# Kernel tuning notes

Hardware: AMD Instinct MI355X
Metric: run time of the kernel (lower is better)

The kernel has to match this reference:

```python
import jax, jax.numpy as jnp
import numpy as np

B, C, T, H = 16, 128, 128, 128


def setup_inputs() -> dict:
    key = jax.random.key(0)
    ks = jax.random.split(key, 9)
    inp = {
        "food_relation": jax.random.normal(ks[0], (B, C, H), jnp.float32),
        "thorn_relation": jax.random.normal(ks[1], (B, C, T, H), jnp.float32),
        "clone": jax.random.normal(ks[2], (B, C, H), jnp.float32),
        "clone_relation": jax.random.normal(ks[3], (B, C, C, H), jnp.float32),
        "thorn_mask": jax.random.randint(ks[4], (B, T), 0, 2, jnp.int32),
        "clone_mask": jax.random.randint(ks[5], (B, C), 0, 2, jnp.int32),
        # MLP(layer_num=1) == Linear(in, h) + activation (ReLU)
        "W_thorn": jax.random.normal(ks[6], (2 * H, H), jnp.float32) / np.sqrt(2 * H),
        "b_thorn": jnp.zeros((H,), jnp.float32),
        "W_clone": jax.random.normal(ks[7], (3 * H, H), jnp.float32) / np.sqrt(3 * H),
        "b_clone": jnp.zeros((H,), jnp.float32),
        "W_agg": jax.random.normal(ks[8], (4 * H, H), jnp.float32) / np.sqrt(4 * H),
        "b_agg": jnp.zeros((H,), jnp.float32),
    }
    return inp


def reference(food_relation, thorn_relation, clone, clone_relation,
              thorn_mask, clone_mask,
              W_thorn, b_thorn, W_clone, b_clone, W_agg, b_agg):
    b, c, h = clone.shape
    t = thorn_relation.shape[2]
    tm = thorn_mask.astype(clone.dtype)[:, None, :, None]  # (b,1,t,1)
    cm = clone_mask.astype(clone.dtype)[:, None, :, None]  # (b,1,c,1)

    # thorn branch: MLP(concat([clone_i, thorn_rel_ij], -1))
    # == clone @ W[:h] (broadcast over t) + rel @ W[h:], avoiding the big concat
    x = ((clone @ W_thorn[:h])[:, :, None, :]
         + jnp.einsum('bcth,hk->bctk', thorn_relation, W_thorn[h:])
         + b_thorn)  # (b,c,t,h)
    thorn_agg = jnp.max(jax.nn.relu(x) * tm, axis=2)  # (b,c,h)

    # clone branch: MLP(concat([clone_i, clone_j, clone_rel_ij], -1))
    y = ((clone @ W_clone[:h])[:, :, None, :]
         + (clone @ W_clone[h:2 * h])[:, None, :, :]
         + jnp.einsum('bcdh,hk->bcdk', clone_relation, W_clone[2 * h:])
         + b_clone)  # (b,c,c,h)
    clone_agg = jnp.max(jax.nn.relu(y) * cm, axis=2)  # (b,c,h)

    agg = jnp.concatenate([clone, food_relation, thorn_agg, clone_agg], axis=-1)  # (b,c,4h)
    return clone + jax.nn.relu(agg @ W_agg + b_agg)
```

## Files before the change

kernel.cpp:

```cpp
#include <hip/hip_runtime.h>

#define BB 16
#define CC 128
#define TT 128
#define HH 128
#define BC (BB*CC)

typedef __attribute__((ext_vector_type(8))) short bf16x8;
typedef __attribute__((ext_vector_type(4))) float f32x4;

__device__ __forceinline__ unsigned short f2bf(float f) {
  union { float f; unsigned u; } v; v.f = f;
  unsigned u = v.u;
  u += 0x7FFFu + ((u >> 16) & 1u);
  return (unsigned short)(u >> 16);
}

__device__ __forceinline__ bf16x8 pack8(f32x4 a, f32x4 b) {
  bf16x8 r;
  r[0] = (short)f2bf(a[0]); r[1] = (short)f2bf(a[1]);
  r[2] = (short)f2bf(a[2]); r[3] = (short)f2bf(a[3]);
  r[4] = (short)f2bf(b[0]); r[5] = (short)f2bf(b[1]);
  r[6] = (short)f2bf(b[2]); r[7] = (short)f2bf(b[3]);
  return r;
}

__device__ __forceinline__ float bf2f(unsigned short u) {
  union { unsigned u; float f; } v; v.u = ((unsigned)u) << 16; return v.f;
}

__global__ __launch_bounds__(256) void prep_kernel(
    const float* __restrict__ Wt, const float* __restrict__ Wc, const float* __restrict__ Wa,
    const float* __restrict__ clone, const float* __restrict__ food,
    const float* __restrict__ bt, const float* __restrict__ bcl,
    const int* __restrict__ tmask, const int* __restrict__ cmask,
    unsigned short* __restrict__ W2sw, unsigned short* __restrict__ Wcsw,
    unsigned short* __restrict__ WaggT,
    float* __restrict__ cpt, float* __restrict__ cp1, float* __restrict__ cj2,
    unsigned short* __restrict__ agg,
    int* __restrict__ tidx, int* __restrict__ tcnt,
    int* __restrict__ cidx, int* __restrict__ ccnt) {
  const int blk = blockIdx.x, tid = threadIdx.x;
  if (blk < 48) {
    int i = blk * 256 + tid;
    if (i < 2048) {
      int f = i >> 6, l = i & 63;
      int kt = f >> 3, n = f & 7;
      int ncol = n * 16 + (l & 15);
      int k0 = kt * 32 + (l >> 4) * 8;
      unsigned short o[8];
      #pragma unroll
      for (int e = 0; e < 8; ++e) o[e] = f2bf(Wt[(128 + k0 + e) * 128 + ncol]);
      *(uint4*)&W2sw[i * 8] = *(uint4*)o;
    } else if (i < 4096) {
      int j = i - 2048;
      int f = j >> 6, l = j & 63;
      int kt = f >> 3, n = f & 7;
      int ncol = n * 16 + (l & 15);
      int k0 = kt * 32 + (l >> 4) * 8;
      unsigned short o[8];
      #pragma unroll
      for (int e = 0; e < 8; ++e) o[e] = f2bf(Wc[(256 + k0 + e) * 128 + ncol]);
      *(uint4*)&Wcsw[j * 8] = *(uint4*)o;
    } else {
      int j = i - 4096;
      int n = j >> 6, k0 = (j & 63) * 8;
      unsigned short o[8];
      #pragma unroll
      for (int e = 0; e < 8; ++e) o[e] = f2bf(Wa[(k0 + e) * 128 + n]);
      *(uint4*)&WaggT[n * 512 + k0] = *(uint4*)o;
    }
  } else if (blk < 304) {
    const int bc0 = (blk - 48) * 8;
    __shared__ float cl[8][128];
    for (int i = tid; i < 1024; i += 256) cl[i >> 7][i & 127] = clone[bc0 * 128 + i];
    __syncthreads();
    const int k = tid & 127, r0 = (tid >> 7) * 4;
    float s1[4], s2[4], s3[4];
    #pragma unroll
    for (int r = 0; r < 4; ++r) { s1[r] = bt[k]; s2[r] = bcl[k]; s3[r] = 0.f; }
    #pragma unroll 4
    for (int h = 0; h < 128; ++h) {
      float w1 = Wt[h * 128 + k], w2 = Wc[h * 128 + k], w3 = Wc[(128 + h) * 128 + k];
      #pragma unroll
      for (int r = 0; r < 4; ++r) {
        float c = cl[r0 + r][h];
        s1[r] = fmaf(c, w1, s1[r]);
        s2[r] = fmaf(c, w2, s2[r]);
        s3[r] = fmaf(c, w3, s3[r]);
      }
    }
    #pragma unroll
    for (int r = 0; r < 4; ++r) {
      cpt[(bc0 + r0 + r) * 128 + k] = s1[r];
      cp1[(bc0 + r0 + r) * 128 + k] = s2[r];
      cj2[(bc0 + r0 + r) * 128 + k] = s3[r];
    }
    for (int i = tid; i < 1024; i += 256) {
      int r = i >> 7, kk = i & 127;
      agg[(size_t)(bc0 + r) * 512 + kk]       = f2bf(cl[r][kk]);
      agg[(size_t)(bc0 + r) * 512 + 128 + kk] = f2bf(food[bc0 * 128 + i]);
    }
  } else {
    if (tid < 32) {
      int b = tid >> 1, which = tid & 1;
      const int* m = which ? cmask : tmask;
      int* idx = which ? cidx : tidx;
      int c = 0;
      for (int i = 0; i < 128; ++i)
        if (m[b * 128 + i]) idx[b * 128 + c++] = i;
      if (which) ccnt[b] = c; else tcnt[b] = c;
    }
  }
}

__global__ __launch_bounds__(512, 4) void branch13(
    const float* __restrict__ trel, const float* __restrict__ crel,
    const float* __restrict__ cpt, const float* __restrict__ cp1,
    const float* __restrict__ cj2,
    const int* __restrict__ tidx, const int* __restrict__ tcnt,
    const int* __restrict__ cidx, const int* __restrict__ ccnt,
    const uint4* __restrict__ W2sw, const uint4* __restrict__ Wcsw,
    unsigned short* __restrict__ agg) {
  __shared__ uint4 Wlds[32 * 64];
  __shared__ unsigned short cj2l[128][130];
  __shared__ int idxl[128];

  const bool isClone = blockIdx.x < 256;
  const int tileIdx = blockIdx.x & 255;
  const float* __restrict__ rel     = isClone ? crel  : trel;
  const float* __restrict__ biasrow = isClone ? cp1   : cpt;
  const int*   __restrict__ idxg    = isClone ? cidx  : tidx;
  const uint4* __restrict__ Wsw     = isClone ? Wcsw  : W2sw;
  const int aggoff = isClone ? 384 : 256;

  const int tid = threadIdx.x;
  const int wave = tid >> 6, lane = tid & 63;
  const int l16 = lane & 15, lk = lane >> 4;
  const int bc0 = tileIdx << 3;
  const int b = bc0 >> 7;
  const int cnt = (isClone ? ccnt : tcnt)[b];
  const int cl  = cnt > 0 ? cnt : 1;

  for (int i = tid; i < 2048; i += 512) Wlds[i] = Wsw[i];
  if (tid < 128) idxl[tid] = idxg[b * 128 + tid];
  if (isClone) {
    const float* cg = cj2 + (size_t)b * 128 * 128;
    for (int i = tid; i < 2048; i += 512) {
      int r = i >> 4, c8 = (i & 15) * 8;
      f32x4 a0 = *(const f32x4*)(cg + r * 128 + c8);
      f32x4 a1 = *(const f32x4*)(cg + r * 128 + c8 + 4);
      bf16x8 p = pack8(a0, a1);
      #pragma unroll
      for (int e = 0; e < 8; ++e) cj2l[c8 + e][r] = (unsigned short)p[e];
    }
  }
  __syncthreads();

  const int bc = bc0 + wave;
  const float* Rb = rel + (size_t)bc * 16384 + lk * 8;

  float bias[8];
  #pragma unroll
  for (int n = 0; n < 8; ++n) bias[n] = biasrow[bc * 128 + n * 16 + l16];

  float vmax[8];
  #pragma unroll
  for (int n = 0; n < 8; ++n) vmax[n] = 0.f;

  #pragma unroll 1
  for (int rg = 0; rg < 8; ++rg) {
    if ((rg << 4) < cnt) {
      int rs = (rg << 4) + l16; if (rs >= cl) rs = cl - 1;
      const float* Rt = Rb + idxl[rs] * 128;
      bf16x8 afr[4];
      #pragma unroll
      for (int kt = 0; kt < 4; ++kt)
        afr[kt] = pack8(*(const f32x4*)(Rt + kt * 32),
                        *(const f32x4*)(Rt + kt * 32 + 4));

      f32x4 acc[8];
      #pragma unroll
      for (int n = 0; n < 8; ++n) acc[n] = (f32x4){0.f, 0.f, 0.f, 0.f};
      #pragma unroll
      for (int kt = 0; kt < 4; ++kt) {
        #pragma unroll
        for (int n = 0; n < 8; ++n) {
          bf16x8 bfr = *(const bf16x8*)&Wlds[(kt * 8 + n) * 64 + lane];
          acc[n] = __builtin_amdgcn_mfma_f32_16x16x32_bf16(afr[kt], bfr, acc[n], 0, 0, 0);
        }
      }

      if (isClone) {
        int rowj[4];
        #pragma unroll
        for (int j = 0; j < 4; ++j) {
          int rj = (rg << 4) + lk * 4 + j; if (rj >= cl) rj = cl - 1;
          rowj[j] = idxl[rj];
        }
        #pragma unroll
        for (int n = 0; n < 8; ++n) {
          const int col = n * 16 + l16;
          #pragma unroll
          for (int j = 0; j < 4; ++j) {
            float x = acc[n][j] + bias[n] + bf2f(cj2l[col][rowj[j]]);
            vmax[n] = fmaxf(vmax[n], fmaxf(x, 0.f));
          }
        }
      } else {
        #pragma unroll
        for (int n = 0; n < 8; ++n) {
          #pragma unroll
          for (int j = 0; j < 4; ++j)
            vmax[n] = fmaxf(vmax[n], fmaxf(acc[n][j] + bias[n], 0.f));
        }
      }
    }
  }

  unsigned short* aggw = agg + (size_t)bc * 512 + aggoff;
  #pragma unroll
  for (int n = 0; n < 8; ++n) {
    float v = vmax[n];
    v = fmaxf(v, __shfl_xor(v, 16));
    v = fmaxf(v, __shfl_xor(v, 32));
    if (lane < 16) aggw[n * 16 + lane] = f2bf(v);
  }
}

__global__ __launch_bounds__(256) void final_kernel(
    const unsigned short* __restrict__ agg, const unsigned short* __restrict__ WaggT,
    const float* __restrict__ clone, const float* __restrict__ bagg,
    float* __restrict__ out) {
  const int tid = threadIdx.x;
  const int wave = tid >> 6, lane = tid & 63;
  const int l16 = lane & 15, lk = lane >> 4;
  const int mrow = blockIdx.x * 16;

  f32x4 acc[2];
  acc[0] = (f32x4){0.f, 0.f, 0.f, 0.f};
  acc[1] = (f32x4){0.f, 0.f, 0.f, 0.f};
  #pragma unroll
  for (int kt = 0; kt < 16; ++kt) {
    bf16x8 a = *(const bf16x8*)(agg + (size_t)(mrow + l16) * 512 + kt * 32 + lk * 8);
    #pragma unroll
    for (int nn = 0; nn < 2; ++nn) {
      int ncol = (wave * 2 + nn) * 16 + l16;
      bf16x8 bfr = *(const bf16x8*)(WaggT + (size_t)ncol * 512 + kt * 32 + lk * 8);
      acc[nn] = __builtin_amdgcn_mfma_f32_16x16x32_bf16(a, bfr, acc[nn], 0, 0, 0);
    }
  }
  #pragma unroll
  for (int nn = 0; nn < 2; ++nn) {
    int col = (wave * 2 + nn) * 16 + l16;
    float bias = bagg[col];
    #pragma unroll
    for (int j = 0; j < 4; ++j) {
      int row = mrow + lk * 4 + j;
      out[row * 128 + col] = clone[row * 128 + col] + fmaxf(acc[nn][j] + bias, 0.f);
    }
  }
}

extern "C" void kernel_launch(void* const* d_in, const int* in_sizes, int n_in,
                              void* d_out, int out_size, void* d_ws, size_t ws_size,
                              hipStream_t stream) {
  const float* food  = (const float*)d_in[0];
  const float* trel  = (const float*)d_in[1];
  const float* clone = (const float*)d_in[2];
  const float* crel  = (const float*)d_in[3];
  const int*   tmask = (const int*)d_in[4];
  const int*   cmask = (const int*)d_in[5];
  const float* Wt    = (const float*)d_in[6];
  const float* bt    = (const float*)d_in[7];
  const float* Wc    = (const float*)d_in[8];
  const float* bcl   = (const float*)d_in[9];
  const float* Wa    = (const float*)d_in[10];
  const float* ba    = (const float*)d_in[11];
  float* out = (float*)d_out;

  char* w = (char*)d_ws;
  float* cpt = (float*)w;                      w += (size_t)BC * 128 * 4;
  float* cp1 = (float*)w;                      w += (size_t)BC * 128 * 4;
  float* cj2 = (float*)w;                      w += (size_t)BC * 128 * 4;
  unsigned short* W2sw  = (unsigned short*)w;  w += 32 * 64 * 8 * 2;
  unsigned short* Wcsw  = (unsigned short*)w;  w += 32 * 64 * 8 * 2;
  unsigned short* WaggT = (unsigned short*)w;  w += 128 * 512 * 2;
  unsigned short* aggb  = (unsigned short*)w;  w += (size_t)BC * 512 * 2;
  int* tidx = (int*)w;                         w += 16 * 128 * 4;
  int* cidx = (int*)w;                         w += 16 * 128 * 4;
  int* tcnt = (int*)w;                         w += 16 * 4;
  int* ccnt = (int*)w;                         w += 16 * 4;

  prep_kernel<<<305, 256, 0, stream>>>(Wt, Wc, Wa, clone, food, bt, bcl,
                                       tmask, cmask,
                                       W2sw, Wcsw, WaggT, cpt, cp1, cj2, aggb,
                                       tidx, tcnt, cidx, ccnt);
  branch13<<<512, 512, 0, stream>>>(trel, crel, cpt, cp1, cj2,
                                    tidx, tcnt, cidx, ccnt,
                                    (const uint4*)W2sw, (const uint4*)Wcsw, aggb);
  final_kernel<<<128, 256, 0, stream>>>(aggb, WaggT, clone, ba, out);
}
```

Baseline: 69.41 us.

## Double-buffer relation rows via global_load_lds and pre-transpose clone projection to bf16

The branch kernel now streams the gathered relation rows straight into LDS with global_load_lds and double-buffers them, so the load of the next 16-row group overlaps with the MFMA work on the current one. The prep kernel writes the clone-j projection already transposed and padded in bf16, so the branch kernel only copies it instead of converting and transposing fp32 data. Blocks shrink to 4 waves and the grid doubles to 1024. The extra 64KB LDS buffer limits occupancy (launch bounds min 1 block), and prefetch correctness depends on manual vmcnt waits.

```diff
diff --git a/kernel.cpp b/kernel.cpp
--- a/kernel.cpp
+++ b/kernel.cpp
@@ -29,6 +29,12 @@
   union { unsigned u; float f; } v; v.u = ((unsigned)u) << 16; return v.f;
 }
 
+__device__ __forceinline__ void gl2lds16(const float* g, uint4* l) {
+  __builtin_amdgcn_global_load_lds(
+      (const __attribute__((address_space(1))) void*)g,
+      (__attribute__((address_space(3))) void*)l, 16, 0, 0);
+}
+
 __global__ __launch_bounds__(256) void prep_kernel(
     const float* __restrict__ Wt, const float* __restrict__ Wc, const float* __restrict__ Wa,
     const float* __restrict__ clone, const float* __restrict__ food,
@@ -36,7 +42,8 @@
     const int* __restrict__ tmask, const int* __restrict__ cmask,
     unsigned short* __restrict__ W2sw, unsigned short* __restrict__ Wcsw,
     unsigned short* __restrict__ WaggT,
-    float* __restrict__ cpt, float* __restrict__ cp1, float* __restrict__ cj2,
+    float* __restrict__ cpt, float* __restrict__ cp1,
+    unsigned short* __restrict__ cj2T,
     unsigned short* __restrict__ agg,
     int* __restrict__ tidx, int* __restrict__ tcnt,
     int* __restrict__ cidx, int* __restrict__ ccnt) {
@@ -90,11 +97,13 @@
         s3[r] = fmaf(c, w3, s3[r]);
       }
     }
+    unsigned short* ct = cj2T + (size_t)(bc0 >> 7) * 16640;
+    const int bl = (bc0 & 127) + r0;
     #pragma unroll
     for (int r = 0; r < 4; ++r) {
       cpt[(bc0 + r0 + r) * 128 + k] = s1[r];
       cp1[(bc0 + r0 + r) * 128 + k] = s2[r];
-      cj2[(bc0 + r0 + r) * 128 + k] = s3[r];
+      ct[k * 130 + bl + r] = f2bf(s3[r]);
     }
     for (int i = tid; i < 1024; i += 256) {
       int r = i >> 7, kk = i & 127;
@@ -114,20 +123,21 @@
   }
 }
 
-__global__ __launch_bounds__(512, 4) void branch13(
+__global__ __launch_bounds__(256, 1) void branch15(
     const float* __restrict__ trel, const float* __restrict__ crel,
     const float* __restrict__ cpt, const float* __restrict__ cp1,
-    const float* __restrict__ cj2,
+    const unsigned short* __restrict__ cj2T,
     const int* __restrict__ tidx, const int* __restrict__ tcnt,
     const int* __restrict__ cidx, const int* __restrict__ ccnt,
     const uint4* __restrict__ W2sw, const uint4* __restrict__ Wcsw,
     unsigned short* __restrict__ agg) {
-  __shared__ uint4 Wlds[32 * 64];
-  __shared__ unsigned short cj2l[128][130];
+  __shared__ uint4 Wlds[2048];
+  __shared__ unsigned short cj2l[128 * 130];
   __shared__ int idxl[128];
-
-  const bool isClone = blockIdx.x < 256;
-  const int tileIdx = blockIdx.x & 255;
+  __shared__ uint4 Abuf[4096];
+
+  const bool isClone = blockIdx.x < 512;
+  const int tileIdx = blockIdx.x & 511;
   const float* __restrict__ rel     = isClone ? crel  : trel;
   const float* __restrict__ biasrow = isClone ? cp1   : cpt;
   const int*   __restrict__ idxg    = isClone ? cidx  : tidx;
@@ -137,29 +147,33 @@
   const int tid = threadIdx.x;
   const int wave = tid >> 6, lane = tid & 63;
   const int l16 = lane & 15, lk = lane >> 4;
-  const int bc0 = tileIdx << 3;
+  const int bc0 = tileIdx << 2;
   const int b = bc0 >> 7;
   const int cnt = (isClone ? ccnt : tcnt)[b];
   const int cl  = cnt > 0 ? cnt : 1;
-
-  for (int i = tid; i < 2048; i += 512) Wlds[i] = Wsw[i];
+  const int nact = (cnt + 15) >> 4;
+
+  const int bc = bc0 + wave;
+  const float* Rb = rel + (size_t)bc * 16384;
+  const int ABASE = wave * 1024;
+
+  if (nact > 0) {
+    int rs0 = l16 < cl ? l16 : cl - 1;
+    const float* rowp = Rb + (size_t)idxg[b * 128 + rs0] * 128 + lk * 8;
+    #pragma unroll
+    for (int q = 0; q < 8; ++q)
+      gl2lds16(rowp + (q >> 1) * 32 + (q & 1) * 4, &Abuf[ABASE + q * 64]);
+  }
+
+  for (int i = tid; i < 2048; i += 256) Wlds[i] = Wsw[i];
   if (tid < 128) idxl[tid] = idxg[b * 128 + tid];
   if (isClone) {
-    const float* cg = cj2 + (size_t)b * 128 * 128;
-    for (int i = tid; i < 2048; i += 512) {
-      int r = i >> 4, c8 = (i & 15) * 8;
-      f32x4 a0 = *(const f32x4*)(cg + r * 128 + c8);
-      f32x4 a1 = *(const f32x4*)(cg + r * 128 + c8 + 4);
-      bf16x8 p = pack8(a0, a1);
-      #pragma unroll
-      for (int e = 0; e < 8; ++e) cj2l[c8 + e][r] = (unsigned short)p[e];
-    }
+    const uint4* cg = (const uint4*)(cj2T + (size_t)b * 16640);
+    uint4* cd = (uint4*)cj2l;
+    for (int i = tid; i < 2080; i += 256) cd[i] = cg[i];
   }
   __syncthreads();
 
-  const int bc = bc0 + wave;
-  const float* Rb = rel + (size_t)bc * 16384 + lk * 8;
-
   float bias[8];
   #pragma unroll
   for (int n = 0; n < 8; ++n) bias[n] = biasrow[bc * 128 + n * 16 + l16];
@@ -169,51 +183,66 @@
   for (int n = 0; n < 8; ++n) vmax[n] = 0.f;
 
   #pragma unroll 1
-  for (int rg = 0; rg < 8; ++rg) {
-    if ((rg << 4) < cnt) {
-      int rs = (rg << 4) + l16; if (rs >= cl) rs = cl - 1;
-      const float* Rt = Rb + idxl[rs] * 128;
-      bf16x8 afr[4];
-      #pragma unroll
-      for (int kt = 0; kt < 4; ++kt)
-        afr[kt] = pack8(*(const f32x4*)(Rt + kt * 32),
-                        *(const f32x4*)(Rt + kt * 32 + 4));
-
-      f32x4 acc[8];
-      #pragma unroll
-      for (int n = 0; n < 8; ++n) acc[n] = (f32x4){0.f, 0.f, 0.f, 0.f};
-      #pragma unroll
-      for (int kt = 0; kt < 4; ++kt) {
-        #pragma unroll
-        for (int n = 0; n < 8; ++n) {
-          bf16x8 bfr = *(const bf16x8*)&Wlds[(kt * 8 + n) * 64 + lane];
-          acc[n] = __builtin_amdgcn_mfma_f32_16x16x32_bf16(afr[kt], bfr, acc[n], 0, 0, 0);
-        }
-      }
-
-      if (isClone) {
-        int rowj[4];
+  for (int i = 0; i < nact; ++i) {
+    const int cur = i & 1;
+    const bool more = (i + 1 < nact);
+
+    if (more) {
+      int rs = ((i + 1) << 4) + l16; if (rs >= cl) rs = cl - 1;
+      const float* rowp = Rb + (size_t)idxl[rs] * 128 + lk * 8;
+      const int nb = ABASE + ((i + 1) & 1) * 512;
+      #pragma unroll
+      for (int q = 0; q < 8; ++q)
+        gl2lds16(rowp + (q >> 1) * 32 + (q & 1) * 4, &Abuf[nb + q * 64]);
+      asm volatile("s_waitcnt vmcnt(8)" ::: "memory");
+    } else {
+      asm volatile("s_waitcnt vmcnt(0)" ::: "memory");
+    }
+    __builtin_amdgcn_sched_barrier(0);
+
+    const int rb = ABASE + cur * 512 + lane;
+    bf16x8 afr[4];
+    #pragma unroll
+    for (int kt = 0; kt < 4; ++kt) {
+      f32x4 a0 = *(const f32x4*)&Abuf[rb + (2 * kt) * 64];
+      f32x4 a1 = *(const f32x4*)&Abuf[rb + (2 * kt + 1) * 64];
+      afr[kt] = pack8(a0, a1);
+    }
+
+    f32x4 acc[8];
+    #pragma unroll
+    for (int n = 0; n < 8; ++n) acc[n] = (f32x4){0.f, 0.f, 0.f, 0.f};
+    #pragma unroll
+    for (int kt = 0; kt < 4; ++kt) {
+      #pragma unroll
+      for (int n = 0; n < 8; ++n) {
+        bf16x8 bfr = *(const bf16x8*)&Wlds[(kt * 8 + n) * 64 + lane];
+        acc[n] = __builtin_amdgcn_mfma_f32_16x16x32_bf16(afr[kt], bfr, acc[n], 0, 0, 0);
+      }
+    }
+
+    if (isClone) {
+      int rowj[4];
+      #pragma unroll
+      for (int j = 0; j < 4; ++j) {
+        int rj = (i << 4) + lk * 4 + j; if (rj >= cl) rj = cl - 1;
+        rowj[j] = idxl[rj];
+      }
+      #pragma unroll
+      for (int n = 0; n < 8; ++n) {
+        const int col = n * 16 + l16;
         #pragma unroll
         for (int j = 0; j < 4; ++j) {
-          int rj = (rg << 4) + lk * 4 + j; if (rj >= cl) rj = cl - 1;
-          rowj[j] = idxl[rj];
+          float x = acc[n][j] + bias[n] + bf2f(cj2l[col * 130 + rowj[j]]);
+          vmax[n] = fmaxf(vmax[n], fmaxf(x, 0.f));
         }
+      }
+    } else {
+      #pragma unroll
+      for (int n = 0; n < 8; ++n) {
         #pragma unroll
-        for (int n = 0; n < 8; ++n) {
-          const int col = n * 16 + l16;
-          #pragma unroll
-          for (int j = 0; j < 4; ++j) {
-            float x = acc[n][j] + bias[n] + bf2f(cj2l[col][rowj[j]]);
-            vmax[n] = fmaxf(vmax[n], fmaxf(x, 0.f));
-          }
-        }
-      } else {
-        #pragma unroll
-        for (int n = 0; n < 8; ++n) {
-          #pragma unroll
-          for (int j = 0; j < 4; ++j)
-            vmax[n] = fmaxf(vmax[n], fmaxf(acc[n][j] + bias[n], 0.f));
-        }
+        for (int j = 0; j < 4; ++j)
+          vmax[n] = fmaxf(vmax[n], fmaxf(acc[n][j] + bias[n], 0.f));
       }
     }
   }
@@ -282,7 +311,7 @@
   char* w = (char*)d_ws;
   float* cpt = (float*)w;                      w += (size_t)BC * 128 * 4;
   float* cp1 = (float*)w;                      w += (size_t)BC * 128 * 4;
-  float* cj2 = (float*)w;                      w += (size_t)BC * 128 * 4;
+  unsigned short* cj2T  = (unsigned short*)w;  w += (size_t)16 * 16640 * 2;
   unsigned short* W2sw  = (unsigned short*)w;  w += 32 * 64 * 8 * 2;
   unsigned short* Wcsw  = (unsigned short*)w;  w += 32 * 64 * 8 * 2;
   unsigned short* WaggT = (unsigned short*)w;  w += 128 * 512 * 2;
@@ -294,10 +323,10 @@
 
   prep_kernel<<<305, 256, 0, stream>>>(Wt, Wc, Wa, clone, food, bt, bcl,
                                        tmask, cmask,
-                                       W2sw, Wcsw, WaggT, cpt, cp1, cj2, aggb,
+                                       W2sw, Wcsw, WaggT, cpt, cp1, cj2T, aggb,
                                        tidx, tcnt, cidx, ccnt);
-  branch13<<<512, 512, 0, stream>>>(trel, crel, cpt, cp1, cj2,
-                                    tidx, tcnt, cidx, ccnt,
-                                    (const uint4*)W2sw, (const uint4*)Wcsw, aggb);
+  branch15<<<1024, 256, 0, stream>>>(trel, crel, cpt, cp1, cj2T,
+                                     tidx, tcnt, cidx, ccnt,
+                                     (const uint4*)W2sw, (const uint4*)Wcsw, aggb);
   final_kernel<<<128, 256, 0, stream>>>(aggb, WaggT, clone, ba, out);
 }
```

New measurement: 97.78 us. 40.9% more time.

## Split branch kernel by output-column halves and precompute transposed bf16 clone term

Applied to the files above, without the earlier changes.

The branch kernel now launches 2048 blocks of 256 threads. Each block handles 4 clone rows and one 64-column half of the output, with a smaller LDS weight slice and fewer accumulators per wave. The prep kernel writes the clone_j projection directly as a transposed, padded bf16 table in global memory, so the branch kernel no longer converts and transposes it into LDS. The aim is more blocks and occupancy and less per-block setup. The cost is that each relation row is now loaded and converted by two blocks, and the clone_j term is read with scattered global loads instead of from LDS.

```diff
diff --git a/kernel.cpp b/kernel.cpp
--- a/kernel.cpp
+++ b/kernel.cpp
@@ -36,7 +36,8 @@
     const int* __restrict__ tmask, const int* __restrict__ cmask,
     unsigned short* __restrict__ W2sw, unsigned short* __restrict__ Wcsw,
     unsigned short* __restrict__ WaggT,
-    float* __restrict__ cpt, float* __restrict__ cp1, float* __restrict__ cj2,
+    float* __restrict__ cpt, float* __restrict__ cp1,
+    unsigned short* __restrict__ cj2T,
     unsigned short* __restrict__ agg,
     int* __restrict__ tidx, int* __restrict__ tcnt,
     int* __restrict__ cidx, int* __restrict__ ccnt) {
@@ -90,11 +91,13 @@
         s3[r] = fmaf(c, w3, s3[r]);
       }
     }
+    unsigned short* ct = cj2T + (size_t)(bc0 >> 7) * 16640;
+    const int bl = (bc0 & 127) + r0;
     #pragma unroll
     for (int r = 0; r < 4; ++r) {
       cpt[(bc0 + r0 + r) * 128 + k] = s1[r];
       cp1[(bc0 + r0 + r) * 128 + k] = s2[r];
-      cj2[(bc0 + r0 + r) * 128 + k] = s3[r];
+      ct[k * 130 + bl + r] = f2bf(s3[r]);
     }
     for (int i = tid; i < 1024; i += 256) {
       int r = i >> 7, kk = i & 127;
@@ -114,20 +117,21 @@
   }
 }
 
-__global__ __launch_bounds__(512, 4) void branch13(
+__global__ __launch_bounds__(256, 8) void branch17(
     const float* __restrict__ trel, const float* __restrict__ crel,
     const float* __restrict__ cpt, const float* __restrict__ cp1,
-    const float* __restrict__ cj2,
+    const unsigned short* __restrict__ cj2T,
     const int* __restrict__ tidx, const int* __restrict__ tcnt,
     const int* __restrict__ cidx, const int* __restrict__ ccnt,
     const uint4* __restrict__ W2sw, const uint4* __restrict__ Wcsw,
     unsigned short* __restrict__ agg) {
-  __shared__ uint4 Wlds[32 * 64];
-  __shared__ unsigned short cj2l[128][130];
+  __shared__ uint4 Wlds[1024];
   __shared__ int idxl[128];
 
-  const bool isClone = blockIdx.x < 256;
-  const int tileIdx = blockIdx.x & 255;
+  const int bx = blockIdx.x;
+  const bool isClone = bx < 1024;
+  const int bi = bx & 1023;
+  const int tb = bi >> 1, half = bi & 1;
   const float* __restrict__ rel     = isClone ? crel  : trel;
   const float* __restrict__ biasrow = isClone ? cp1   : cpt;
   const int*   __restrict__ idxg    = isClone ? cidx  : tidx;
@@ -137,36 +141,31 @@
   const int tid = threadIdx.x;
   const int wave = tid >> 6, lane = tid & 63;
   const int l16 = lane & 15, lk = lane >> 4;
-  const int bc0 = tileIdx << 3;
+  const int bc0 = tb << 2;
   const int b = bc0 >> 7;
   const int cnt = (isClone ? ccnt : tcnt)[b];
   const int cl  = cnt > 0 ? cnt : 1;
 
-  for (int i = tid; i < 2048; i += 512) Wlds[i] = Wsw[i];
+  for (int i = tid; i < 1024; i += 256) {
+    int fl = i >> 6, l = i & 63;
+    int kt = fl >> 2, nl = fl & 3;
+    Wlds[i] = Wsw[(kt * 8 + half * 4 + nl) * 64 + l];
+  }
   if (tid < 128) idxl[tid] = idxg[b * 128 + tid];
-  if (isClone) {
-    const float* cg = cj2 + (size_t)b * 128 * 128;
-    for (int i = tid; i < 2048; i += 512) {
-      int r = i >> 4, c8 = (i & 15) * 8;
-      f32x4 a0 = *(const f32x4*)(cg + r * 128 + c8);
-      f32x4 a1 = *(const f32x4*)(cg + r * 128 + c8 + 4);
-      bf16x8 p = pack8(a0, a1);
-      #pragma unroll
-      for (int e = 0; e < 8; ++e) cj2l[c8 + e][r] = (unsigned short)p[e];
-    }
-  }
   __syncthreads();
 
   const int bc = bc0 + wave;
   const float* Rb = rel + (size_t)bc * 16384 + lk * 8;
-
-  float bias[8];
-  #pragma unroll
-  for (int n = 0; n < 8; ++n) bias[n] = biasrow[bc * 128 + n * 16 + l16];
-
-  float vmax[8];
-  #pragma unroll
-  for (int n = 0; n < 8; ++n) vmax[n] = 0.f;
+  const unsigned short* cjb = cj2T + (size_t)b * 16640;
+
+  float bias[4];
+  #pragma unroll
+  for (int n = 0; n < 4; ++n)
+    bias[n] = biasrow[bc * 128 + half * 64 + n * 16 + l16];
+
+  float vmax[4];
+  #pragma unroll
+  for (int n = 0; n < 4; ++n) vmax[n] = 0.f;
 
   #pragma unroll 1
   for (int rg = 0; rg < 8; ++rg) {
@@ -179,14 +178,14 @@
         afr[kt] = pack8(*(const f32x4*)(Rt + kt * 32),
                         *(const f32x4*)(Rt + kt * 32 + 4));
 
-      f32x4 acc[8];
-      #pragma unroll
-      for (int n = 0; n < 8; ++n) acc[n] = (f32x4){0.f, 0.f, 0.f, 0.f};
+      f32x4 acc[4];
+      #pragma unroll
+      for (int n = 0; n < 4; ++n) acc[n] = (f32x4){0.f, 0.f, 0.f, 0.f};
       #pragma unroll
       for (int kt = 0; kt < 4; ++kt) {
         #pragma unroll
-        for (int n = 0; n < 8; ++n) {
-          bf16x8 bfr = *(const bf16x8*)&Wlds[(kt * 8 + n) * 64 + lane];
+        for (int n = 0; n < 4; ++n) {
+          bf16x8 bfr = *(const bf16x8*)&Wlds[(kt * 4 + n) * 64 + lane];
           acc[n] = __builtin_amdgcn_mfma_f32_16x16x32_bf16(afr[kt], bfr, acc[n], 0, 0, 0);
         }
       }
@@ -199,17 +198,17 @@
           rowj[j] = idxl[rj];
         }
         #pragma unroll
-        for (int n = 0; n < 8; ++n) {
-          const int col = n * 16 + l16;
+        for (int n = 0; n < 4; ++n) {
+          const int col = half * 64 + n * 16 + l16;
           #pragma unroll
           for (int j = 0; j < 4; ++j) {
-            float x = acc[n][j] + bias[n] + bf2f(cj2l[col][rowj[j]]);
+            float x = acc[n][j] + bias[n] + bf2f(cjb[col * 130 + rowj[j]]);
             vmax[n] = fmaxf(vmax[n], fmaxf(x, 0.f));
           }
         }
       } else {
         #pragma unroll
-        for (int n = 0; n < 8; ++n) {
+        for (int n = 0; n < 4; ++n) {
           #pragma unroll
           for (int j = 0; j < 4; ++j)
             vmax[n] = fmaxf(vmax[n], fmaxf(acc[n][j] + bias[n], 0.f));
@@ -218,9 +217,9 @@
     }
   }
 
-  unsigned short* aggw = agg + (size_t)bc * 512 + aggoff;
-  #pragma unroll
-  for (int n = 0; n < 8; ++n) {
+  unsigned short* aggw = agg + (size_t)bc * 512 + aggoff + half * 64;
+  #pragma unroll
+  for (int n = 0; n < 4; ++n) {
     float v = vmax[n];
     v = fmaxf(v, __shfl_xor(v, 16));
     v = fmaxf(v, __shfl_xor(v, 32));
@@ -282,7 +281,7 @@
   char* w = (char*)d_ws;
   float* cpt = (float*)w;                      w += (size_t)BC * 128 * 4;
   float* cp1 = (float*)w;                      w += (size_t)BC * 128 * 4;
-  float* cj2 = (float*)w;                      w += (size_t)BC * 128 * 4;
+  unsigned short* cj2T  = (unsigned short*)w;  w += (size_t)16 * 16640 * 2;
   unsigned short* W2sw  = (unsigned short*)w;  w += 32 * 64 * 8 * 2;
   unsigned short* Wcsw  = (unsigned short*)w;  w += 32 * 64 * 8 * 2;
   unsigned short* WaggT = (unsigned short*)w;  w += 128 * 512 * 2;
@@ -294,10 +293,10 @@
 
   prep_kernel<<<305, 256, 0, stream>>>(Wt, Wc, Wa, clone, food, bt, bcl,
                                        tmask, cmask,
-                                       W2sw, Wcsw, WaggT, cpt, cp1, cj2, aggb,
+                                       W2sw, Wcsw, WaggT, cpt, cp1, cj2T, aggb,
                                        tidx, tcnt, cidx, ccnt);
-  branch13<<<512, 512, 0, stream>>>(trel, crel, cpt, cp1, cj2,
-                                    tidx, tcnt, cidx, ccnt,
-                                    (const uint4*)W2sw, (const uint4*)Wcsw, aggb);
+  branch17<<<2048, 256, 0, stream>>>(trel, crel, cpt, cp1, cj2T,
+                                     tidx, tcnt, cidx, ccnt,
+                                     (const uint4*)W2sw, (const uint4*)Wcsw, aggb);
   final_kernel<<<128, 256, 0, stream>>>(aggb, WaggT, clone, ba, out);
 }
```

After: 89.66 us. 29.2% more time.

## Pre-transpose clone projection to bf16 in prep and stage relation rows via LDS

Applied to the files above, without the earlier changes.

The prep kernel now writes the clone_j projection as a transposed, padded bf16 table in global memory, so the branch kernel no longer loads, converts and transposes a 128x128 fp32 tile into shared memory in every block. The branch kernel reads that table directly from global memory (served by cache). Relation rows are now loaded with coalesced 16-byte per-lane reads, converted with the hardware bf16 conversion and staged through a per-wave LDS buffer before forming the MFMA A fragments. The per-element ReLU clamp is dropped because vmax starts at zero. Risks include extra LDS traffic, uncoalesced gathers from the cj2T table, and a change in rounding behaviour from the library bf16 conversion.

```diff
diff --git a/kernel.cpp b/kernel.cpp
--- a/kernel.cpp
+++ b/kernel.cpp
@@ -1,4 +1,5 @@
 #include <hip/hip_runtime.h>
+#include <hip/hip_bf16.h>
 
 #define BB 16
 #define CC 128
@@ -7,6 +8,7 @@
 #define BC (BB*CC)
 
 typedef __attribute__((ext_vector_type(8))) short bf16x8;
+typedef __attribute__((ext_vector_type(4))) short bf16x4;
 typedef __attribute__((ext_vector_type(4))) float f32x4;
 
 __device__ __forceinline__ unsigned short f2bf(float f) {
@@ -16,12 +18,11 @@
   return (unsigned short)(u >> 16);
 }
 
-__device__ __forceinline__ bf16x8 pack8(f32x4 a, f32x4 b) {
-  bf16x8 r;
-  r[0] = (short)f2bf(a[0]); r[1] = (short)f2bf(a[1]);
-  r[2] = (short)f2bf(a[2]); r[3] = (short)f2bf(a[3]);
-  r[4] = (short)f2bf(b[0]); r[5] = (short)f2bf(b[1]);
-  r[6] = (short)f2bf(b[2]); r[7] = (short)f2bf(b[3]);
+__device__ __forceinline__ bf16x4 pack4hw(f32x4 a) {
+  union { __hip_bfloat16 h; short s; } c;
+  bf16x4 r;
+  #pragma unroll
+  for (int e = 0; e < 4; ++e) { c.h = __float2bfloat16(a[e]); r[e] = c.s; }
   return r;
 }
 
@@ -36,7 +37,8 @@
     const int* __restrict__ tmask, const int* __restrict__ cmask,
     unsigned short* __restrict__ W2sw, unsigned short* __restrict__ Wcsw,
     unsigned short* __restrict__ WaggT,
-    float* __restrict__ cpt, float* __restrict__ cp1, float* __restrict__ cj2,
+    float* __restrict__ cpt, float* __restrict__ cp1,
+    unsigned short* __restrict__ cj2T,
     unsigned short* __restrict__ agg,
     int* __restrict__ tidx, int* __restrict__ tcnt,
     int* __restrict__ cidx, int* __restrict__ ccnt) {
@@ -90,11 +92,13 @@
         s3[r] = fmaf(c, w3, s3[r]);
       }
     }
+    unsigned short* ct = cj2T + (size_t)(bc0 >> 7) * 16640;
+    const int bl = (bc0 & 127) + r0;
     #pragma unroll
     for (int r = 0; r < 4; ++r) {
       cpt[(bc0 + r0 + r) * 128 + k] = s1[r];
       cp1[(bc0 + r0 + r) * 128 + k] = s2[r];
-      cj2[(bc0 + r0 + r) * 128 + k] = s3[r];
+      ct[k * 130 + bl + r] = f2bf(s3[r]);
     }
     for (int i = tid; i < 1024; i += 256) {
       int r = i >> 7, kk = i & 127;
@@ -114,16 +118,16 @@
   }
 }
 
-__global__ __launch_bounds__(512, 4) void branch13(
+__global__ __launch_bounds__(512, 4) void branch19(
     const float* __restrict__ trel, const float* __restrict__ crel,
     const float* __restrict__ cpt, const float* __restrict__ cp1,
-    const float* __restrict__ cj2,
+    const unsigned short* __restrict__ cj2T,
     const int* __restrict__ tidx, const int* __restrict__ tcnt,
     const int* __restrict__ cidx, const int* __restrict__ ccnt,
     const uint4* __restrict__ W2sw, const uint4* __restrict__ Wcsw,
     unsigned short* __restrict__ agg) {
-  __shared__ uint4 Wlds[32 * 64];
-  __shared__ unsigned short cj2l[128][130];
+  __shared__ uint4 Wlds[2048];
+  __shared__ unsigned short Astg[8][16][136];
   __shared__ int idxl[128];
 
   const bool isClone = blockIdx.x < 256;
@@ -137,6 +141,7 @@
   const int tid = threadIdx.x;
   const int wave = tid >> 6, lane = tid & 63;
   const int l16 = lane & 15, lk = lane >> 4;
+  const int l8 = lane & 7, lo = lane >> 3;
   const int bc0 = tileIdx << 3;
   const int b = bc0 >> 7;
   const int cnt = (isClone ? ccnt : tcnt)[b];
@@ -144,21 +149,11 @@
 
   for (int i = tid; i < 2048; i += 512) Wlds[i] = Wsw[i];
   if (tid < 128) idxl[tid] = idxg[b * 128 + tid];
-  if (isClone) {
-    const float* cg = cj2 + (size_t)b * 128 * 128;
-    for (int i = tid; i < 2048; i += 512) {
-      int r = i >> 4, c8 = (i & 15) * 8;
-      f32x4 a0 = *(const f32x4*)(cg + r * 128 + c8);
-      f32x4 a1 = *(const f32x4*)(cg + r * 128 + c8 + 4);
-      bf16x8 p = pack8(a0, a1);
-      #pragma unroll
-      for (int e = 0; e < 8; ++e) cj2l[c8 + e][r] = (unsigned short)p[e];
-    }
-  }
   __syncthreads();
 
   const int bc = bc0 + wave;
-  const float* Rb = rel + (size_t)bc * 16384 + lk * 8;
+  const float* Rb = rel + (size_t)bc * 16384;
+  const unsigned short* cjb = cj2T + (size_t)b * 16640;
 
   float bias[8];
   #pragma unroll
@@ -171,13 +166,20 @@
   #pragma unroll 1
   for (int rg = 0; rg < 8; ++rg) {
     if ((rg << 4) < cnt) {
-      int rs = (rg << 4) + l16; if (rs >= cl) rs = cl - 1;
-      const float* Rt = Rb + idxl[rs] * 128;
+      #pragma unroll
+      for (int q = 0; q < 8; ++q) {
+        const int rl = (q & 1) * 8 + lo;
+        int rs = (rg << 4) + rl; if (rs >= cl) rs = cl - 1;
+        const float* src = Rb + (size_t)idxl[rs] * 128 + (q >> 1) * 32 + l8 * 4;
+        f32x4 v = *(const f32x4*)src;
+        const int c16 = (q >> 1) * 8 + l8;
+        *(bf16x4*)&Astg[wave][rl][c16 * 4] = pack4hw(v);
+      }
+
       bf16x8 afr[4];
       #pragma unroll
       for (int kt = 0; kt < 4; ++kt)
-        afr[kt] = pack8(*(const f32x4*)(Rt + kt * 32),
-                        *(const f32x4*)(Rt + kt * 32 + 4));
+        afr[kt] = *(const bf16x8*)&Astg[wave][l16][kt * 32 + lk * 8];
 
       f32x4 acc[8];
       #pragma unroll
@@ -203,8 +205,8 @@
           const int col = n * 16 + l16;
           #pragma unroll
           for (int j = 0; j < 4; ++j) {
-            float x = acc[n][j] + bias[n] + bf2f(cj2l[col][rowj[j]]);
-            vmax[n] = fmaxf(vmax[n], fmaxf(x, 0.f));
+            float x = acc[n][j] + bias[n] + bf2f(cjb[col * 130 + rowj[j]]);
+            vmax[n] = fmaxf(vmax[n], x);
           }
         }
       } else {
@@ -212,7 +214,7 @@
         for (int n = 0; n < 8; ++n) {
           #pragma unroll
           for (int j = 0; j < 4; ++j)
-            vmax[n] = fmaxf(vmax[n], fmaxf(acc[n][j] + bias[n], 0.f));
+            vmax[n] = fmaxf(vmax[n], acc[n][j] + bias[n]);
         }
       }
     }
@@ -282,7 +284,7 @@
   char* w = (char*)d_ws;
   float* cpt = (float*)w;                      w += (size_t)BC * 128 * 4;
   float* cp1 = (float*)w;                      w += (size_t)BC * 128 * 4;
-  float* cj2 = (float*)w;                      w += (size_t)BC * 128 * 4;
+  unsigned short* cj2T  = (unsigned short*)w;  w += (size_t)16 * 16640 * 2;
   unsigned short* W2sw  = (unsigned short*)w;  w += 32 * 64 * 8 * 2;
   unsigned short* Wcsw  = (unsigned short*)w;  w += 32 * 64 * 8 * 2;
   unsigned short* WaggT = (unsigned short*)w;  w += 128 * 512 * 2;
@@ -294,9 +296,9 @@
 
   prep_kernel<<<305, 256, 0, stream>>>(Wt, Wc, Wa, clone, food, bt, bcl,
                                        tmask, cmask,
-                                       W2sw, Wcsw, WaggT, cpt, cp1, cj2, aggb,
+                                       W2sw, Wcsw, WaggT, cpt, cp1, cj2T, aggb,
                                        tidx, tcnt, cidx, ccnt);
-  branch13<<<512, 512, 0, stream>>>(trel, crel, cpt, cp1, cj2,
+  branch19<<<512, 512, 0, stream>>>(trel, crel, cpt, cp1, cj2T,
                                     tidx, tcnt, cidx, ccnt,
                                     (const uint4*)W2sw, (const uint4*)Wcsw, aggb);
   final_kernel<<<128, 256, 0, stream>>>(aggb, WaggT, clone, ba, out);
```

New measurement: 76.22 us. 1.1x slower.
